# Optimization experiments

Hardware: AMD Instinct MI355X
Metric: run time of the kernel (lower is better)

Reference implementation:

```python
import jax, jax.numpy as jnp
import numpy as np

B, N, DIN, U, K, DEG = 64, 512, 256, 128, 2, 8
BN = B * N
E = BN * DEG
D4 = 4 * U
HEADS = 2


def setup_inputs() -> dict:
    key = jax.random.key(0)
    ks = jax.random.split(key, 24)
    rng = np.random.default_rng(0)
    # block-diagonal batched graph: each of B graphs has N nodes, N*DEG random edges
    src = rng.integers(0, N, size=(B, N * DEG))
    dst = rng.integers(0, N, size=(B, N * DEG))
    off = (np.arange(B) * N)[:, None]
    edge_index = jnp.asarray(np.stack([(src + off).reshape(-1), (dst + off).reshape(-1)]), dtype=jnp.int32)

    def w(k, shape, fan):
        return (jax.random.normal(k, shape, dtype=jnp.float32) / np.sqrt(fan)).astype(jnp.float32)

    gin = (DIN + U) * (K + 1)  # gconv concatenates K+1 hop features of concat([x, h])
    inp = dict(
        x_od=jax.random.normal(ks[0], (BN, DIN), dtype=jnp.float32),
        history=jax.random.normal(ks[1], (BN, DIN), dtype=jnp.float32),
        yesterday=jax.random.normal(ks[2], (BN, DIN), dtype=jnp.float32),
        edge_index=edge_index,
        edge_weight=jax.random.uniform(ks[3], (E,), dtype=jnp.float32),
        W_ru_f=w(ks[4], (gin, 2 * U), gin), b_ru_f=jnp.zeros((2 * U,), jnp.float32),
        W_c_f=w(ks[5], (gin, U), gin), b_c_f=jnp.zeros((U,), jnp.float32),
        W_ru_l=w(ks[6], (gin, 2 * U), gin), b_ru_l=jnp.zeros((2 * U,), jnp.float32),
        W_c_l=w(ks[7], (gin, U), gin), b_c_l=jnp.zeros((U,), jnp.float32),
        W_ru_s=w(ks[8], (gin, 2 * U), gin), b_ru_s=jnp.zeros((2 * U,), jnp.float32),
        W_c_s=w(ks[9], (gin, U), gin), b_c_s=jnp.zeros((U,), jnp.float32),
        W_hd=w(ks[10], (D4, 2 * U), 2 * U), b_hd=jnp.zeros((D4,), jnp.float32),
        W_in=w(ks[11], (3 * D4, D4), D4), b_in=jnp.zeros((3 * D4,), jnp.float32),
        W_out=w(ks[12], (D4, D4), D4), b_out=jnp.zeros((D4,), jnp.float32),
        W_gate=w(ks[13], (U, D4), D4), b_gate=jnp.zeros((U,), jnp.float32),
    )
    return inp


def _gconv(x, src, dst, ew, W, b):
    # K-hop mean-normalized graph convolution over the batched edge list
    num = x.shape[0]
    deg = jnp.maximum(jax.ops.segment_sum(ew, dst, num_segments=num), 1.0)[:, None]
    feats = [x]
    h = x
    for _ in range(K):
        h = jax.ops.segment_sum(h[src] * ew[:, None], dst, num_segments=num) / deg
        feats.append(h)
    return jnp.concatenate(feats, axis=-1) @ W + b


def _ggru(x, h, src, dst, ew, W_ru, b_ru, W_c, b_c):
    ru = jax.nn.sigmoid(_gconv(jnp.concatenate([x, h], -1), src, dst, ew, W_ru, b_ru))
    r, u = jnp.split(ru, 2, axis=-1)
    c = jnp.tanh(_gconv(jnp.concatenate([x, r * h], -1), src, dst, ew, W_c, b_c))
    return u * h + (1.0 - u) * c


def _pos_enc(seq_len, d):
    pos = jnp.arange(seq_len, dtype=jnp.float32)[:, None]
    div = jnp.exp(jnp.arange(0, d, 2, dtype=jnp.float32) * (-jnp.log(10000.0) / d))
    pe = jnp.zeros((seq_len, d), jnp.float32)
    pe = pe.at[:, 0::2].set(jnp.sin(pos * div)).at[:, 1::2].set(jnp.cos(pos * div))
    return pe  # (seq_len, d)


def reference(x_od, history, yesterday, edge_index, edge_weight,
              W_ru_f, b_ru_f, W_c_f, b_c_f,
              W_ru_l, b_ru_l, W_c_l, b_c_l,
              W_ru_s, b_ru_s, W_c_s, b_c_s,
              W_hd, b_hd, W_in, b_in, W_out, b_out, W_gate, b_gate):
    src, dst = edge_index[0], edge_index[1]
    ew = edge_weight
    h0 = jnp.zeros((BN, U), jnp.float32)
    hf = _ggru(x_od, h0, src, dst, ew, W_ru_f, b_ru_f, W_c_f, b_c_f)      # finished branch
    hl = _ggru(history, h0, src, dst, ew, W_ru_l, b_ru_l, W_c_l, b_c_l)  # long-history branch
    hs = _ggru(yesterday, h0, src, dst, ew, W_ru_s, b_ru_s, W_c_s, b_c_s)  # short-history branch
    # hidden fusion: raw view(-1, 2U, N) as in the torch source
    fusion = jnp.concatenate([hs, hl], axis=-1).reshape(B, 2 * U, N)
    uh = jnp.einsum('oc,bcn->bon', W_hd, fusion) + b_hd[:, None]  # (B, 4U, N)
    uh = uh + _pos_enc(B, D4)[:, :, None]                          # pos-enc over batch dim, as in source
    x = uh.transpose(2, 0, 1)                                      # (N, B, 4U): seq=N, batch=B
    # multi-head self-attention (torch MultiheadAttention semantics)
    qkv = x @ W_in.T + b_in
    q, k_, v = jnp.split(qkv, 3, axis=-1)
    hd = D4 // HEADS
    qh = q.reshape(N, B, HEADS, hd)
    kh = k_.reshape(N, B, HEADS, hd)
    vh = v.reshape(N, B, HEADS, hd)
    scores = jnp.einsum('sbhd,tbhd->bhst', qh, kh) / jnp.sqrt(jnp.float32(hd))
    attn = jax.nn.softmax(scores, axis=-1)
    ctx = jnp.einsum('bhst,tbhd->sbhd', attn, vh).reshape(N, B, D4)
    attn_out = ctx @ W_out.T + b_out                               # (N, B, 4U)
    gated = jnp.einsum('oc,bcn->bon', W_gate, attn_out.transpose(1, 2, 0)) + b_gate[:, None]  # (B, U, N)
    attn_flat = gated.transpose(0, 2, 1).reshape(BN, U)
    # (enc_first_out==finished_hidden, long_hidden, short_hidden, gated attention)
    return jnp.stack([hf, hl, hs, attn_flat])
```

## Files before the change

kernel.cpp:

```cpp
#include <hip/hip_runtime.h>
#include <hip/hip_bf16.h>
#include <math.h>


#define DEV __device__ __forceinline__

typedef __attribute__((ext_vector_type(4))) float  f32x4;
typedef __attribute__((ext_vector_type(4))) float  fvec4;
typedef __attribute__((ext_vector_type(8))) short  bf16x8;
typedef __attribute__((ext_vector_type(4))) unsigned short u16x4;

constexpr int BN_ = 32768;
constexpr int E_  = 262144;
constexpr long OUTSEC = 4194304;

DEV unsigned short f2bf(float f){
  union { float f; unsigned u; } v; v.f = f;
  unsigned r = (v.u + 0x7FFFu + ((v.u >> 16) & 1u)) >> 16;
  return (unsigned short)r;
}
DEV float b2f(unsigned short h){
  union { unsigned u; float f; } v; v.u = ((unsigned)h) << 16;
  return v.f;
}

__global__ __launch_bounds__(256) void histdeg_kernel(const int* __restrict__ ei,
    const float* __restrict__ ew, unsigned* __restrict__ cnt, float* __restrict__ deg){
  int e = blockIdx.x*256 + threadIdx.x;
  int d = ei[E_ + e];
  atomicAdd(&cnt[d], 1u);
  atomicAdd(&deg[d], ew[e]);
}

__global__ __launch_bounds__(1024) void scan_kernel(const unsigned* __restrict__ cnt,
                                                    unsigned* __restrict__ rowptr){
  __shared__ unsigned sm[1024];
  __shared__ unsigned carry;
  int tid = threadIdx.x;
  if (tid == 0) carry = 0;
  __syncthreads();
  for (int base = 0; base < BN_; base += 1024){
    unsigned v = cnt[base + tid];
    sm[tid] = v;
    __syncthreads();
    for (int off = 1; off < 1024; off <<= 1){
      unsigned t = (tid >= off) ? sm[tid - off] : 0u;
      __syncthreads();
      sm[tid] += t;
      __syncthreads();
    }
    rowptr[base + tid] = carry + sm[tid] - v;
    __syncthreads();
    if (tid == 1023) carry += sm[1023];
    __syncthreads();
  }
  if (tid == 0) rowptr[BN_] = carry;
}

__global__ __launch_bounds__(256) void scatter_kernel(const int* __restrict__ ei,
    const float* __restrict__ ew, const unsigned* __restrict__ rowptr,
    unsigned* __restrict__ curs, unsigned* __restrict__ csrc, float* __restrict__ csrw){
  int e = blockIdx.x*256 + threadIdx.x;
  int d = ei[E_ + e];
  unsigned pos = atomicAdd(&curs[d], 1u);
  unsigned idx = rowptr[d] + pos;
  csrc[idx] = (unsigned)ei[e];
  csrw[idx] = ew[e];
}

template<int SRC>
__global__ __launch_bounds__(256) void prop_kernel(const float* __restrict__ xf,
    const unsigned short* __restrict__ zin, unsigned short* __restrict__ zout,
    const unsigned* __restrict__ rowptr, const unsigned* __restrict__ csrc,
    const float* __restrict__ csrw, const float* __restrict__ deg){
  int node = blockIdx.x*4 + (threadIdx.x >> 6);
  int l = threadIdx.x & 63;
  unsigned b0 = rowptr[node], b1 = rowptr[node + 1];
  float a0 = 0.f, a1 = 0.f, a2 = 0.f, a3 = 0.f;
  for (unsigned e = b0; e < b1; ++e){
    int s = csrc[e]; float w = csrw[e];
    if constexpr (SRC == 0){
      fvec4 v = *(const fvec4*)(xf + (long)s*256 + l*4);
      a0 += w*v[0]; a1 += w*v[1]; a2 += w*v[2]; a3 += w*v[3];
    } else {
      u16x4 v = *(const u16x4*)(zin + (long)s*768 + l*4);
      a0 += w*b2f(v[0]); a1 += w*b2f(v[1]); a2 += w*b2f(v[2]); a3 += w*b2f(v[3]);
    }
  }
  float dg = deg[node]; dg = dg > 1.f ? dg : 1.f;
  float inv = 1.f / dg;
  u16x4 o = { f2bf(a0*inv), f2bf(a1*inv), f2bf(a2*inv), f2bf(a3*inv) };
  *(u16x4*)(zout + (long)node*768 + l*4) = o;
}

__global__ __launch_bounds__(256) void convx_kernel(const float* __restrict__ xf,
                                                    unsigned short* __restrict__ zcat){
  int id = blockIdx.x*256 + threadIdx.x;
  fvec4 v = ((const fvec4*)xf)[id];
  int m = id >> 6, c4 = id & 63;
  u16x4 o = { f2bf(v[0]), f2bf(v[1]), f2bf(v[2]), f2bf(v[3]) };
  *(u16x4*)(zcat + (long)m*768 + c4*4) = o;
}

__global__ __launch_bounds__(256) void cvt_f2b_kernel(const float* __restrict__ s,
                                                      unsigned short* __restrict__ d, int n){
  int i = blockIdx.x*256 + threadIdx.x;
  if (i < n) d[i] = f2bf(s[i]);
}

__global__ __launch_bounds__(256) void tcvt_kernel(const float* __restrict__ s,
    unsigned short* __restrict__ d, int lgC, int R){
  int id = blockIdx.x*256 + threadIdx.x;
  int r = id >> lgC, c = id & ((1 << lgC) - 1);
  d[(long)c*R + r] = f2bf(s[id]);
}

__global__ __launch_bounds__(256) void weff_kernel(const float* __restrict__ Wru,
    const float* __restrict__ bru, const float* __restrict__ Wc, const float* __restrict__ bc,
    unsigned short* __restrict__ Weff, float* __restrict__ beff){
  int id = blockIdx.x*256 + threadIdx.x;
  int n = id / 768, k = id % 768;
  int row = (k >> 8)*384 + (k & 255);
  float w = (n < 128) ? Wru[(long)row*256 + 128 + n] : Wc[(long)row*128 + (n - 128)];
  Weff[(long)n*768 + k] = f2bf(w);
  if (k == 0) beff[n] = (n < 128) ? bru[128 + n] : bc[n - 128];
}

__global__ __launch_bounds__(256) void pe_kernel(const float* __restrict__ bhd,
                                                 float* __restrict__ PET4){
  int id = blockIdx.x*256 + threadIdx.x;
  int b = id >> 9, o = id & 511;
  float j2 = (float)(o & ~1);
  float ang = (float)b * expf(-j2 * (9.210340371976184f / 512.f));
  float v = ((o & 1) ? cosf(ang) : sinf(ang)) + bhd[o];
  PET4[(o >> 2)*256 + b*4 + (o & 3)] = v;
}

__global__ __launch_bounds__(256) void peq2_kernel(const float* __restrict__ Win,
    const float* __restrict__ bin, const float* __restrict__ PET4, float* __restrict__ peq2){
  int j = blockIdx.x*4 + (threadIdx.x >> 6);
  int l = threadIdx.x & 63;
  float acc = 0.f;
  for (int o4 = 0; o4 < 128; ++o4){
    fvec4 wv = *(const fvec4*)(Win + (long)j*512 + o4*4);
    fvec4 pv = *(const fvec4*)(PET4 + o4*256 + l*4);
    acc += wv[0]*pv[0] + wv[1]*pv[1] + wv[2]*pv[2] + wv[3]*pv[3];
  }
  peq2[(long)l*1536 + j] = bin[j] + acc;
}

__global__ __launch_bounds__(128) void beq_kernel(const float* __restrict__ Wgt,
    const float* __restrict__ bout, const float* __restrict__ bgate, float* __restrict__ beq){
  int g = threadIdx.x;
  float s = bgate[g];
  for (int c = 0; c < 512; ++c) s += Wgt[(long)g*512 + c] * bout[c];
  beq[g] = s;
}

template<int MODE, int EPI>
__global__ __launch_bounds__(256) void gemm_bt(
    const unsigned short* __restrict__ A, const unsigned short* __restrict__ Bt,
    float* __restrict__ Cf, unsigned short* __restrict__ Cb,
    int Ktot, int lda, int ldb, int ldc,
    long sA, long sB, long sC, int g0,
    const float* __restrict__ bias, const float* __restrict__ pe, float scale)
{
  __shared__ unsigned short As[128*64];
  __shared__ unsigned short Bs[128*64];
  const int tid = threadIdx.x;
  long aOff, bOff, cOff;
  if constexpr (MODE == 0){
    aOff = blockIdx.z * sA; bOff = blockIdx.z * sB; cOff = blockIdx.z * sC;
  } else if constexpr (MODE == 1){
    int g = g0 + blockIdx.z;
    long base = (long)(g >> 1)*1536 + (long)(g & 1)*256;
    aOff = base; bOff = base + 512; cOff = (long)blockIdx.z * 262144;
  } else {
    int g = g0 + blockIdx.z;
    aOff = (long)blockIdx.z * 262144;
    bOff = (long)g * 131072;
    cOff = (long)g * 256;
  }
  const int bm = blockIdx.y * 128, bn = blockIdx.x * 128;
  const int w = tid >> 6, l = tid & 63;
  const int wr = w >> 1, wc = w & 1;

  const unsigned short* aB[4];
  const unsigned short* bB[4];
  #pragma unroll
  for (int i = 0; i < 4; ++i){
    int c = tid + i*256;
    int row = c >> 3, gg = c & 7;
    aB[i] = A  + aOff + (long)(bm + row)*lda + gg*8;
    bB[i] = Bt + bOff + (long)(bn + row)*ldb + gg*8;
  }

  f32x4 acc[4][4] = {};
  for (int kt = 0; kt < Ktot; kt += 64){
    #pragma unroll
    for (int i = 0; i < 4; ++i){
      __builtin_amdgcn_global_load_lds(
        (const __attribute__((address_space(1))) unsigned int*)(aB[i] + kt),
        (__attribute__((address_space(3))) unsigned int*)&As[(i*256 + w*64)*8], 16, 0, 0);
      __builtin_amdgcn_global_load_lds(
        (const __attribute__((address_space(1))) unsigned int*)(bB[i] + kt),
        (__attribute__((address_space(3))) unsigned int*)&Bs[(i*256 + w*64)*8], 16, 0, 0);
    }
    __syncthreads();
    #pragma unroll
    for (int ks = 0; ks < 2; ++ks){
      bf16x8 aF[4], bF[4];
      #pragma unroll
      for (int mi = 0; mi < 4; ++mi)
        aF[mi] = *(const bf16x8*)(&As[(wr*64 + mi*16 + (l & 15))*64 + ks*32 + (l >> 4)*8]);
      #pragma unroll
      for (int ni = 0; ni < 4; ++ni)
        bF[ni] = *(const bf16x8*)(&Bs[(wc*64 + ni*16 + (l & 15))*64 + ks*32 + (l >> 4)*8]);
      #pragma unroll
      for (int mi = 0; mi < 4; ++mi)
        #pragma unroll
        for (int ni = 0; ni < 4; ++ni)
          acc[mi][ni] = __builtin_amdgcn_mfma_f32_16x16x32_bf16(aF[mi], bF[ni], acc[mi][ni], 0, 0, 0);
    }
    __syncthreads();
  }
  #pragma unroll
  for (int mi = 0; mi < 4; ++mi){
    #pragma unroll
    for (int ni = 0; ni < 4; ++ni){
      int col = bn + wc*64 + ni*16 + (l & 15);
      int row0 = bm + wr*64 + mi*16 + ((l >> 4) << 2);
      #pragma unroll
      for (int j = 0; j < 4; ++j){
        int row = row0 + j;
        float v = acc[mi][ni][j] * scale;
        if (bias) v += bias[col];
        if constexpr (EPI == 5) v += pe[((row & 63) * 1536) + col];
        if constexpr (EPI == 0){
          Cf[cOff + (long)row*ldc + col] = v;
        } else if constexpr (EPI == 4){
          long orow = (long)(row & 63)*512 + (row >> 6);
          Cf[orow*ldc + col] = v;
        } else {
          Cb[cOff + (long)row*ldc + col] = f2bf(v);
        }
      }
    }
  }
}

__global__ __launch_bounds__(256) void ucepi_kernel(const unsigned short* __restrict__ uc,
                                                    float* __restrict__ outp){
  int id = blockIdx.x*256 + threadIdx.x;
  int m = id >> 7, n = id & 127;
  float ul = b2f(uc[(long)m*256 + n]);
  float cl = b2f(uc[(long)m*256 + 128 + n]);
  float u = 1.f / (1.f + expf(-ul));
  outp[id] = (1.f - u) * tanhf(cl);
}

__global__ __launch_bounds__(256) void afus_kernel(const float* __restrict__ out,
                                                   unsigned short* __restrict__ Afus){
  int rc = blockIdx.x, a = blockIdx.y, b = blockIdx.z;
  int c = threadIdx.x;
  const float* hsrc = out + 2*OUTSEC;
  const float* hlrc = out + 1*OUTSEC;
  long rowb = (long)b*512 + 2*c + a;
  #pragma unroll 4
  for (int r0 = 0; r0 < 32; ++r0){
    int r = rc*32 + r0;
    float v = (r < 128) ? hsrc[rowb*128 + r] : hlrc[rowb*128 + (r - 128)];
    long mrow = (long)(a*256 + r)*64 + b;
    Afus[mrow*256 + c] = f2bf(v);
  }
}

__global__ __launch_bounds__(256) void vt_kernel(const unsigned short* __restrict__ qkv,
                                                 unsigned short* __restrict__ vT){
  int g = blockIdx.y; int b = g >> 1, h = g & 1;
  int tt = blockIdx.x & 7, dt = blockIdx.x >> 3;
  __shared__ unsigned short sm[64][65];
  int lrow = threadIdx.x >> 6, lcol = threadIdx.x & 63;
  const unsigned short* src = qkv + (long)b*1536 + 1024 + (long)h*256 + dt*64;
  #pragma unroll
  for (int i = 0; i < 16; ++i){
    int t = tt*64 + lrow + i*4;
    sm[lrow + i*4][lcol] = src[(long)t*98304 + lcol];
  }
  __syncthreads();
  unsigned short* dstp = vT + (long)g*131072 + (long)(dt*64)*512 + tt*64;
  #pragma unroll
  for (int i = 0; i < 16; ++i){
    int d = lrow + i*4;
    dstp[(long)d*512 + lcol] = sm[lcol][d];
  }
}

__global__ __launch_bounds__(256) void softmax_kernel(const float* __restrict__ S,
                                                      unsigned short* __restrict__ P){
  int row = blockIdx.x*4 + (threadIdx.x >> 6);
  int l = threadIdx.x & 63;
  const fvec4* sr = (const fvec4*)(S + (long)row*512);
  fvec4 v0 = sr[l], v1 = sr[l + 64];
  float m = fmaxf(fmaxf(fmaxf(v0[0],v0[1]), fmaxf(v0[2],v0[3])),
                  fmaxf(fmaxf(v1[0],v1[1]), fmaxf(v1[2],v1[3])));
  #pragma unroll
  for (int off = 32; off; off >>= 1) m = fmaxf(m, __shfl_xor(m, off));
  float e0[4], e1[4], s = 0.f;
  #pragma unroll
  for (int j = 0; j < 4; ++j){ e0[j] = expf(v0[j]-m); s += e0[j]; }
  #pragma unroll
  for (int j = 0; j < 4; ++j){ e1[j] = expf(v1[j]-m); s += e1[j]; }
  #pragma unroll
  for (int off = 32; off; off >>= 1) s += __shfl_xor(s, off);
  float inv = 1.f / s;
  u16x4 p0 = { f2bf(e0[0]*inv), f2bf(e0[1]*inv), f2bf(e0[2]*inv), f2bf(e0[3]*inv) };
  u16x4 p1 = { f2bf(e1[0]*inv), f2bf(e1[1]*inv), f2bf(e1[2]*inv), f2bf(e1[3]*inv) };
  *(u16x4*)(P + (long)row*512 + l*4) = p0;
  *(u16x4*)(P + (long)row*512 + 256 + l*4) = p1;
}

extern "C" void kernel_launch(void* const* d_in, const int* in_sizes, int n_in,
                              void* d_out, int out_size, void* d_ws, size_t ws_size,
                              hipStream_t stream)
{
  (void)in_sizes; (void)n_in; (void)out_size;
  constexpr long MB = 1l << 20;
  if (ws_size < 216*MB) return;

  const float* xin[3] = {(const float*)d_in[0], (const float*)d_in[1], (const float*)d_in[2]};
  const int*   ei = (const int*)d_in[3];
  const float* ew = (const float*)d_in[4];
  const float* Wru[3] = {(const float*)d_in[5], (const float*)d_in[9],  (const float*)d_in[13]};
  const float* bru[3] = {(const float*)d_in[6], (const float*)d_in[10], (const float*)d_in[14]};
  const float* Wc[3]  = {(const float*)d_in[7], (const float*)d_in[11], (const float*)d_in[15]};
  const float* bc[3]  = {(const float*)d_in[8], (const float*)d_in[12], (const float*)d_in[16]};
  const float* Whd  = (const float*)d_in[17]; const float* bhd   = (const float*)d_in[18];
  const float* Win  = (const float*)d_in[19]; const float* bin   = (const float*)d_in[20];
  const float* Wout = (const float*)d_in[21]; const float* bout  = (const float*)d_in[22];
  const float* Wgt  = (const float*)d_in[23]; const float* bgate = (const float*)d_in[24];
  float* out = (float*)d_out;
  char* ws = (char*)d_ws;

  float*    deg    = (float*)(ws + 0);
  unsigned* cnt    = (unsigned*)(ws + 131072);
  unsigned* rowptr = (unsigned*)(ws + 262144);
  unsigned* curs   = (unsigned*)(ws + 524288);
  unsigned* csrc   = (unsigned*)(ws + 786432);
  float*    csrw   = (float*)(ws + 1835008);
  unsigned short* Weff = (unsigned short*)(ws + 2883584);
  float*    beff   = (float*)(ws + 4063232);
  float*    beq    = (float*)(ws + 4194304);
  unsigned short* WIN   = (unsigned short*)(ws + 4456448);
  unsigned short* WGTB  = (unsigned short*)(ws + 6029312);
  unsigned short* WHDT  = (unsigned short*)(ws + 6160384);
  unsigned short* WOUTT = (unsigned short*)(ws + 6422528);
  unsigned short* Wq2t  = (unsigned short*)(ws + 6946816);
  unsigned short* Weqt  = (unsigned short*)(ws + 7733248);
  float*    PET4   = (float*)(ws + 7864320);
  float*    PEQ2   = (float*)(ws + 7995392);
  unsigned short* AFUS = (unsigned short*)(ws + 8*MB);
  unsigned short* ZCAT = (unsigned short*)(ws + 40*MB);
  unsigned short* UC   = (unsigned short*)(ws + 88*MB);
  unsigned short* QKV  = (unsigned short*)(ws + 40*MB);
  unsigned short* VT   = (unsigned short*)(ws + 136*MB);
  unsigned short* CTX  = (unsigned short*)(ws + 168*MB);
  float*    SCORES = (float*)(ws + 8*MB);
  unsigned short* PBUF = (unsigned short*)(ws + 200*MB);

  hipMemsetAsync(deg,  0, 131072, stream);
  hipMemsetAsync(cnt,  0, 131072, stream);
  hipMemsetAsync(curs, 0, 131072, stream);
  histdeg_kernel<<<1024, 256, 0, stream>>>(ei, ew, cnt, deg);
  scan_kernel<<<1, 1024, 0, stream>>>(cnt, rowptr);
  scatter_kernel<<<1024, 256, 0, stream>>>(ei, ew, rowptr, curs, csrc, csrw);

  for (int br = 0; br < 3; ++br)
    weff_kernel<<<768, 256, 0, stream>>>(Wru[br], bru[br], Wc[br], bc[br],
                                         Weff + (long)br*196608, beff + br*256);
  cvt_f2b_kernel<<<3072, 256, 0, stream>>>(Win, WIN,  786432);
  cvt_f2b_kernel<<<256,  256, 0, stream>>>(Wgt, WGTB, 65536);
  tcvt_kernel<<<512,  256, 0, stream>>>(Whd,  WHDT,  8, 512);
  tcvt_kernel<<<1024, 256, 0, stream>>>(Wout, WOUTT, 9, 512);
  pe_kernel<<<128, 256, 0, stream>>>(bhd, PET4);

  gemm_bt<0,2><<<dim3(2,12,1), 256, 0, stream>>>(WIN, WHDT, nullptr, Wq2t,
      512, 512, 512, 256, 0,0,0, 0, nullptr, nullptr, 1.0f);
  gemm_bt<0,2><<<dim3(4,1,1), 256, 0, stream>>>(WGTB, WOUTT, nullptr, Weqt,
      512, 512, 512, 512, 0,0,0, 0, nullptr, nullptr, 1.0f);
  peq2_kernel<<<384, 256, 0, stream>>>(Win, bin, PET4, PEQ2);
  beq_kernel<<<1, 128, 0, stream>>>(Wgt, bout, bgate, beq);

  for (int br = 0; br < 3; ++br){
    convx_kernel<<<8192, 256, 0, stream>>>(xin[br], ZCAT);
    prop_kernel<0><<<8192, 256, 0, stream>>>(xin[br], nullptr, ZCAT + 256,
                                             rowptr, csrc, csrw, deg);
    prop_kernel<1><<<8192, 256, 0, stream>>>(nullptr, ZCAT + 256, ZCAT + 512,
                                             rowptr, csrc, csrw, deg);
    gemm_bt<0,2><<<dim3(2,256,1), 256, 0, stream>>>(ZCAT, Weff + (long)br*196608,
        nullptr, UC, 768, 768, 768, 256, 0,0,0, 0, beff + br*256, nullptr, 1.0f);
    ucepi_kernel<<<16384, 256, 0, stream>>>(UC, out + (long)br*OUTSEC);
  }

  afus_kernel<<<dim3(8,2,64), 256, 0, stream>>>(out, AFUS);
  gemm_bt<0,5><<<dim3(12,256,1), 256, 0, stream>>>(AFUS, Wq2t, nullptr, QKV,
      256, 256, 256, 1536, 0,0,0, 0, nullptr, PEQ2, 1.0f);
  vt_kernel<<<dim3(32,128), 256, 0, stream>>>(QKV, VT);

  for (int c4 = 0; c4 < 4; ++c4){
    gemm_bt<1,0><<<dim3(4,4,32), 256, 0, stream>>>(QKV, QKV, SCORES, nullptr,
        256, 98304, 98304, 512, 0,0,0, c4*32, nullptr, nullptr, 0.0625f);
    softmax_kernel<<<4096, 256, 0, stream>>>(SCORES, PBUF);
    gemm_bt<2,2><<<dim3(2,4,32), 256, 0, stream>>>(PBUF, VT, nullptr, CTX,
        512, 512, 512, 32768, 0,0,0, c4*32, nullptr, nullptr, 1.0f);
  }

  gemm_bt<0,4><<<dim3(1,256,1), 256, 0, stream>>>(CTX, Weqt, out + 3*OUTSEC, nullptr,
      512, 512, 512, 128, 0,0,0, 0, beq, nullptr, 1.0f);
}
```

Baseline: 1.042 ms.

## Batch GRU branches into single launches, fuse gate epilogue, bf16 in-place attention scores

```diff
diff --git a/kernel.cpp b/kernel.cpp
--- a/kernel.cpp
+++ b/kernel.cpp
@@ -13,6 +13,7 @@
 constexpr int BN_ = 32768;
 constexpr int E_  = 262144;
 constexpr long OUTSEC = 4194304;
+constexpr long ZSZE = 25165824;
 
 DEV unsigned short f2bf(float f){
   union { float f; unsigned u; } v; v.f = f;
@@ -69,12 +70,17 @@
 }
 
 template<int SRC>
-__global__ __launch_bounds__(256) void prop_kernel(const float* __restrict__ xf,
-    const unsigned short* __restrict__ zin, unsigned short* __restrict__ zout,
+__global__ __launch_bounds__(256) void prop3_kernel(const float* __restrict__ x0,
+    const float* __restrict__ x1, const float* __restrict__ x2,
+    unsigned short* __restrict__ zcat,
     const unsigned* __restrict__ rowptr, const unsigned* __restrict__ csrc,
     const float* __restrict__ csrw, const float* __restrict__ deg){
   int node = blockIdx.x*4 + (threadIdx.x >> 6);
   int l = threadIdx.x & 63;
+  int z = blockIdx.z;
+  const float* xf = (z == 0) ? x0 : (z == 1) ? x1 : x2;
+  const unsigned short* zin = zcat + z*ZSZE + 256;
+  unsigned short* zout = zcat + z*ZSZE + (SRC == 0 ? 256 : 512);
   unsigned b0 = rowptr[node], b1 = rowptr[node + 1];
   float a0 = 0.f, a1 = 0.f, a2 = 0.f, a3 = 0.f;
   for (unsigned e = b0; e < b1; ++e){
@@ -93,13 +99,16 @@
   *(u16x4*)(zout + (long)node*768 + l*4) = o;
 }
 
-__global__ __launch_bounds__(256) void convx_kernel(const float* __restrict__ xf,
-                                                    unsigned short* __restrict__ zcat){
+__global__ __launch_bounds__(256) void convx3_kernel(const float* __restrict__ x0,
+    const float* __restrict__ x1, const float* __restrict__ x2,
+    unsigned short* __restrict__ zcat){
   int id = blockIdx.x*256 + threadIdx.x;
+  int z = blockIdx.z;
+  const float* xf = (z == 0) ? x0 : (z == 1) ? x1 : x2;
   fvec4 v = ((const fvec4*)xf)[id];
   int m = id >> 6, c4 = id & 63;
   u16x4 o = { f2bf(v[0]), f2bf(v[1]), f2bf(v[2]), f2bf(v[3]) };
-  *(u16x4*)(zcat + (long)m*768 + c4*4) = o;
+  *(u16x4*)(zcat + z*ZSZE + (long)m*768 + c4*4) = o;
 }
 
 __global__ __launch_bounds__(256) void cvt_f2b_kernel(const float* __restrict__ s,
@@ -121,9 +130,10 @@
   int id = blockIdx.x*256 + threadIdx.x;
   int n = id / 768, k = id % 768;
   int row = (k >> 8)*384 + (k & 255);
-  float w = (n < 128) ? Wru[(long)row*256 + 128 + n] : Wc[(long)row*128 + (n - 128)];
+  int j = n >> 1;
+  float w = ((n & 1) == 0) ? Wru[(long)row*256 + 128 + j] : Wc[(long)row*128 + j];
   Weff[(long)n*768 + k] = f2bf(w);
-  if (k == 0) beff[n] = (n < 128) ? bru[128 + n] : bc[n - 128];
+  if (k == 0) beff[n] = ((n & 1) == 0) ? bru[128 + j] : bc[j];
 }
 
 __global__ __launch_bounds__(256) void pe_kernel(const float* __restrict__ bhd,
@@ -169,7 +179,7 @@
   __shared__ unsigned short Bs[128*64];
   const int tid = threadIdx.x;
   long aOff, bOff, cOff;
-  if constexpr (MODE == 0){
+  if constexpr (MODE == 0 || MODE == 3){
     aOff = blockIdx.z * sA; bOff = blockIdx.z * sB; cOff = blockIdx.z * sC;
   } else if constexpr (MODE == 1){
     int g = g0 + blockIdx.z;
@@ -234,29 +244,28 @@
       for (int j = 0; j < 4; ++j){
         int row = row0 + j;
         float v = acc[mi][ni][j] * scale;
-        if (bias) v += bias[col];
+        if (bias){
+          if constexpr (MODE == 3) v += bias[(int)blockIdx.z*256 + col];
+          else v += bias[col];
+        }
         if constexpr (EPI == 5) v += pe[((row & 63) * 1536) + col];
         if constexpr (EPI == 0){
           Cf[cOff + (long)row*ldc + col] = v;
         } else if constexpr (EPI == 4){
           long orow = (long)(row & 63)*512 + (row >> 6);
           Cf[orow*ldc + col] = v;
+        } else if constexpr (EPI == 7){
+          float other = __shfl_xor(v, 1);
+          if (!(l & 1)){
+            float uu = 1.f / (1.f + expf(-v));
+            Cf[cOff + (long)row*ldc + (col >> 1)] = (1.f - uu) * tanhf(other);
+          }
         } else {
           Cb[cOff + (long)row*ldc + col] = f2bf(v);
         }
       }
     }
   }
-}
-
-__global__ __launch_bounds__(256) void ucepi_kernel(const unsigned short* __restrict__ uc,
-                                                    float* __restrict__ outp){
-  int id = blockIdx.x*256 + threadIdx.x;
-  int m = id >> 7, n = id & 127;
-  float ul = b2f(uc[(long)m*256 + n]);
-  float cl = b2f(uc[(long)m*256 + 128 + n]);
-  float u = 1.f / (1.f + expf(-ul));
-  outp[id] = (1.f - u) * tanhf(cl);
 }
 
 __global__ __launch_bounds__(256) void afus_kernel(const float* __restrict__ out,
@@ -296,28 +305,29 @@
   }
 }
 
-__global__ __launch_bounds__(256) void softmax_kernel(const float* __restrict__ S,
-                                                      unsigned short* __restrict__ P){
-  int row = blockIdx.x*4 + (threadIdx.x >> 6);
+__global__ __launch_bounds__(256) void smax_kernel(unsigned short* __restrict__ S){
+  long row = (long)blockIdx.x*4 + (threadIdx.x >> 6);
   int l = threadIdx.x & 63;
-  const fvec4* sr = (const fvec4*)(S + (long)row*512);
-  fvec4 v0 = sr[l], v1 = sr[l + 64];
-  float m = fmaxf(fmaxf(fmaxf(v0[0],v0[1]), fmaxf(v0[2],v0[3])),
-                  fmaxf(fmaxf(v1[0],v1[1]), fmaxf(v1[2],v1[3])));
+  unsigned short* p = S + row*512 + l*8;
+  bf16x8 v = *(const bf16x8*)p;
+  float f[8];
+  #pragma unroll
+  for (int j = 0; j < 8; ++j) f[j] = b2f((unsigned short)v[j]);
+  float m = f[0];
+  #pragma unroll
+  for (int j = 1; j < 8; ++j) m = fmaxf(m, f[j]);
   #pragma unroll
   for (int off = 32; off; off >>= 1) m = fmaxf(m, __shfl_xor(m, off));
-  float e0[4], e1[4], s = 0.f;
-  #pragma unroll
-  for (int j = 0; j < 4; ++j){ e0[j] = expf(v0[j]-m); s += e0[j]; }
-  #pragma unroll
-  for (int j = 0; j < 4; ++j){ e1[j] = expf(v1[j]-m); s += e1[j]; }
+  float s = 0.f;
+  #pragma unroll
+  for (int j = 0; j < 8; ++j){ f[j] = expf(f[j] - m); s += f[j]; }
   #pragma unroll
   for (int off = 32; off; off >>= 1) s += __shfl_xor(s, off);
   float inv = 1.f / s;
-  u16x4 p0 = { f2bf(e0[0]*inv), f2bf(e0[1]*inv), f2bf(e0[2]*inv), f2bf(e0[3]*inv) };
-  u16x4 p1 = { f2bf(e1[0]*inv), f2bf(e1[1]*inv), f2bf(e1[2]*inv), f2bf(e1[3]*inv) };
-  *(u16x4*)(P + (long)row*512 + l*4) = p0;
-  *(u16x4*)(P + (long)row*512 + 256 + l*4) = p1;
+  bf16x8 o;
+  #pragma unroll
+  for (int j = 0; j < 8; ++j) o[j] = (short)f2bf(f[j]*inv);
+  *(bf16x8*)p = o;
 }
 
 extern "C" void kernel_launch(void* const* d_in, const int* in_sizes, int n_in,
@@ -326,9 +336,11 @@
 {
   (void)in_sizes; (void)n_in; (void)out_size;
   constexpr long MB = 1l << 20;
-  if (ws_size < 216*MB) return;
-
-  const float* xin[3] = {(const float*)d_in[0], (const float*)d_in[1], (const float*)d_in[2]};
+  if (ws_size < 200*MB) return;
+
+  const float* x0 = (const float*)d_in[0];
+  const float* x1 = (const float*)d_in[1];
+  const float* x2 = (const float*)d_in[2];
   const int*   ei = (const int*)d_in[3];
   const float* ew = (const float*)d_in[4];
   const float* Wru[3] = {(const float*)d_in[5], (const float*)d_in[9],  (const float*)d_in[13]};
@@ -359,14 +371,12 @@
   unsigned short* Weqt  = (unsigned short*)(ws + 7733248);
   float*    PET4   = (float*)(ws + 7864320);
   float*    PEQ2   = (float*)(ws + 7995392);
-  unsigned short* AFUS = (unsigned short*)(ws + 8*MB);
-  unsigned short* ZCAT = (unsigned short*)(ws + 40*MB);
-  unsigned short* UC   = (unsigned short*)(ws + 88*MB);
-  unsigned short* QKV  = (unsigned short*)(ws + 40*MB);
-  unsigned short* VT   = (unsigned short*)(ws + 136*MB);
-  unsigned short* CTX  = (unsigned short*)(ws + 168*MB);
-  float*    SCORES = (float*)(ws + 8*MB);
-  unsigned short* PBUF = (unsigned short*)(ws + 200*MB);
+  unsigned short* ZCAT3 = (unsigned short*)(ws + 40*MB);
+  unsigned short* AFUS  = (unsigned short*)(ws + 8*MB);
+  unsigned short* QKV   = (unsigned short*)(ws + 40*MB);
+  unsigned short* VT    = (unsigned short*)(ws + 8*MB);
+  unsigned short* SCOREB= (unsigned short*)(ws + 136*MB);
+  unsigned short* CTX   = (unsigned short*)(ws + 40*MB);
 
   hipMemsetAsync(deg,  0, 131072, stream);
   hipMemsetAsync(cnt,  0, 131072, stream);
@@ -391,29 +401,24 @@
   peq2_kernel<<<384, 256, 0, stream>>>(Win, bin, PET4, PEQ2);
   beq_kernel<<<1, 128, 0, stream>>>(Wgt, bout, bgate, beq);
 
-  for (int br = 0; br < 3; ++br){
-    convx_kernel<<<8192, 256, 0, stream>>>(xin[br], ZCAT);
-    prop_kernel<0><<<8192, 256, 0, stream>>>(xin[br], nullptr, ZCAT + 256,
-                                             rowptr, csrc, csrw, deg);
-    prop_kernel<1><<<8192, 256, 0, stream>>>(nullptr, ZCAT + 256, ZCAT + 512,
-                                             rowptr, csrc, csrw, deg);
-    gemm_bt<0,2><<<dim3(2,256,1), 256, 0, stream>>>(ZCAT, Weff + (long)br*196608,
-        nullptr, UC, 768, 768, 768, 256, 0,0,0, 0, beff + br*256, nullptr, 1.0f);
-    ucepi_kernel<<<16384, 256, 0, stream>>>(UC, out + (long)br*OUTSEC);
-  }
+  convx3_kernel<<<dim3(8192,1,3), 256, 0, stream>>>(x0, x1, x2, ZCAT3);
+  prop3_kernel<0><<<dim3(8192,1,3), 256, 0, stream>>>(x0, x1, x2, ZCAT3,
+                                                      rowptr, csrc, csrw, deg);
+  prop3_kernel<1><<<dim3(8192,1,3), 256, 0, stream>>>(x0, x1, x2, ZCAT3,
+                                                      rowptr, csrc, csrw, deg);
+  gemm_bt<3,7><<<dim3(2,256,3), 256, 0, stream>>>(ZCAT3, Weff, out, nullptr,
+      768, 768, 768, 128, ZSZE, 196608, OUTSEC, 0, beff, nullptr, 1.0f);
 
   afus_kernel<<<dim3(8,2,64), 256, 0, stream>>>(out, AFUS);
   gemm_bt<0,5><<<dim3(12,256,1), 256, 0, stream>>>(AFUS, Wq2t, nullptr, QKV,
       256, 256, 256, 1536, 0,0,0, 0, nullptr, PEQ2, 1.0f);
   vt_kernel<<<dim3(32,128), 256, 0, stream>>>(QKV, VT);
 
-  for (int c4 = 0; c4 < 4; ++c4){
-    gemm_bt<1,0><<<dim3(4,4,32), 256, 0, stream>>>(QKV, QKV, SCORES, nullptr,
-        256, 98304, 98304, 512, 0,0,0, c4*32, nullptr, nullptr, 0.0625f);
-    softmax_kernel<<<4096, 256, 0, stream>>>(SCORES, PBUF);
-    gemm_bt<2,2><<<dim3(2,4,32), 256, 0, stream>>>(PBUF, VT, nullptr, CTX,
-        512, 512, 512, 32768, 0,0,0, c4*32, nullptr, nullptr, 1.0f);
-  }
+  gemm_bt<1,2><<<dim3(4,4,128), 256, 0, stream>>>(QKV, QKV, nullptr, SCOREB,
+      256, 98304, 98304, 512, 0,0,0, 0, nullptr, nullptr, 0.0625f);
+  smax_kernel<<<16384, 256, 0, stream>>>(SCOREB);
+  gemm_bt<2,2><<<dim3(2,4,128), 256, 0, stream>>>(SCOREB, VT, nullptr, CTX,
+      512, 512, 512, 32768, 0,0,0, 0, nullptr, nullptr, 1.0f);
 
   gemm_bt<0,4><<<dim3(1,256,1), 256, 0, stream>>>(CTX, Weqt, out + 3*OUTSEC, nullptr,
       512, 512, 512, 128, 0,0,0, 0, beq, nullptr, 1.0f);
```

Result: faster. 993.2 us (-4.7%).
